# Optimization experiments

Hardware: AMD Instinct MI355X
Metric: run time of the kernel (lower is better)

## Reference

```python
import jax, jax.numpy as jnp
import numpy as np

# dims: T=max seq len, B=batch, D=d_embed, H=d_hidden, NR=n_roles, NH=n_heads
T, B, D, H = 512, 64, 512, 1024
NR, NH = 64, 8
HD = H // NH  # per-head hidden


def _lengths():
    # monotonically non-increasing lengths -> valid PackedSequence batch_sizes
    return np.round(np.linspace(T, T // 4, B)).astype(np.int32)


def _packed_idx(lengths):
    batch_sizes = np.array([(lengths > t).sum() for t in range(T)], dtype=np.int64)
    # flat row index into padded [T*B] for each packed token (time-major)
    return np.concatenate([t * B + np.arange(batch_sizes[t]) for t in range(T)]).astype(np.int32)


def setup_inputs() -> dict:
    key = jax.random.key(0)
    ks = jax.random.split(key, 12)
    lengths = _lengths()
    idx = _packed_idx(lengths)
    total = int(idx.shape[0])  # 20480
    s = lambda k, shape, sc=1.0: (jax.random.normal(k, shape, jnp.float32) * sc)
    return {
        'x': s(ks[0], (total, D)),
        'idx': jnp.asarray(idx),
        'lengths': jnp.asarray(lengths),
        'basis0': s(ks[1], (NR, H)),  # frozen role basis (requires_grad=False)
        'basis1': s(ks[2], (NR, H)),
        'Wx0': s(ks[3], (2 * H, D), 0.02), 'bx0': jnp.zeros((2 * H,), jnp.float32),
        'Wh0': s(ks[4], (2 * H, H), 0.02), 'bh0': jnp.zeros((2 * H,), jnp.float32),
        'Wv0': s(ks[5], (2 * H, H), 0.02), 'bv0': jnp.zeros((2 * H,), jnp.float32),
        'Wx1': s(ks[6], (2 * H, H), 0.02), 'bx1': jnp.zeros((2 * H,), jnp.float32),
        'Wh1': s(ks[7], (2 * H, H), 0.02), 'bh1': jnp.zeros((2 * H,), jnp.float32),
        'Wv1': s(ks[8], (2 * H, H), 0.02), 'bv1': jnp.zeros((2 * H,), jnp.float32),
    }


def _tpru_layer(x2fg_pad, Wh, bh, r, u, lengths):
    """Run the sequential TPRU recurrence over padded [T,B,2H] precomputed x2fg.

    Replaces the packed per-timestep Python loop (output[p:q] slicing with
    varying batch sizes) with a full-batch lax.scan; rows of padded timesteps
    beyond a sequence's length are computed but never read into output or hn,
    so the math on valid positions is identical.
    """
    h0 = jnp.zeros((B, H), x2fg_pad.dtype)
    hn0 = jnp.zeros((B, H), x2fg_pad.dtype)

    def step(carry, inp):
        h, hn = carry
        x2fg_t, t = inp
        fg = h @ Wh.T + bh + x2fg_t                 # [B, 2H]
        f, g = jnp.split(fg, 2, axis=-1)
        fh = f.reshape(B, NH, HD)
        # unbind: attention over roles per head
        scores = jnp.einsum('bnd,rnd->brn', fh, r)   # [B, NR, NH]
        attn = jax.nn.softmax(scores, axis=1)
        # bind: weighted sum of unbinding vectors
        bind = jnp.einsum('brn,rnd->bnd', attn, u).reshape(B, H)
        gate = jax.nn.sigmoid(g)
        h_new = gate * jnp.tanh(bind) + (1.0 - gate) * h
        # hn captures hidden at each sequence's final valid step
        hn = jnp.where((lengths == t + 1)[:, None], h_new, hn)
        return (h_new, hn), h_new

    (_, hn), hs = jax.lax.scan(step, (h0, hn0), (x2fg_pad, jnp.arange(T)))
    return hs, hn  # hs: [T, B, H]


def reference(x, idx, lengths, basis0, basis1, Wx0, bx0, Wh0, bh0, Wv0, bv0,
              Wx1, bx1, Wh1, bh1, Wv1, bv1):
    # unpack packed data [total, D] into padded [T, B, D]
    x_pad = jnp.zeros((T * B, D), x.dtype).at[idx].set(x).reshape(T, B, D)
    # layer 0
    x2fg = x_pad @ Wx0.T + bx0                       # [T, B, 2H]
    v = (basis0 @ Wv0.T + bv0).reshape(NR, NH, 2 * HD)
    hs, hn0 = _tpru_layer(x2fg, Wh0, bh0, v[..., :HD], v[..., HD:], lengths)
    # layer 1 (input dim is now H)
    x2fg = hs @ Wx1.T + bx1
    v = (basis1 @ Wv1.T + bv1).reshape(NR, NH, 2 * HD)
    hs, hn1 = _tpru_layer(x2fg, Wh1, bh1, v[..., :HD], v[..., HD:], lengths)
    # repack output (time-major packed order, matching PackedSequence.data)
    packed = hs.reshape(T * B, H)[idx]               # [total, H]
    hn = jnp.stack([hn0, hn1])                       # [n_layers, B, H]
    return packed, hn
```

## Files before the change

### kernel.cpp

```cpp
#include <hip/hip_runtime.h>

typedef _Float16 f16;
typedef _Float16 f16x2 __attribute__((ext_vector_type(2)));
typedef _Float16 f16x4 __attribute__((ext_vector_type(4)));
typedef _Float16 f16x8 __attribute__((ext_vector_type(8)));
typedef float    f32x4 __attribute__((ext_vector_type(4)));

#define TT   512
#define BB   64
#define DD   512
#define HH   1024
#define H2   2048
#define NR_  64
#define NH_  8
#define HD_  128
#define MROWS (TT*BB)
#define RWG  64

#define ALOAD32(p)   __hip_atomic_load((p),  __ATOMIC_RELAXED, __HIP_MEMORY_SCOPE_AGENT)
#define ASTORE(p,v)  __hip_atomic_store((p), (v), __ATOMIC_RELAXED, __HIP_MEMORY_SCOPE_AGENT)

__global__ void k_cvt(const float* __restrict__ s, f16* __restrict__ d, int n) {
  int i = blockIdx.x * blockDim.x + threadIdx.x;
  int st = gridDim.x * blockDim.x;
  for (; i < n; i += st) d[i] = (f16)s[i];
}

__global__ void k_scatter(const float* __restrict__ x, const int* __restrict__ idx,
                          f16* __restrict__ xpad, int total) {
  int i = blockIdx.x * blockDim.x + threadIdx.x;
  int st = gridDim.x * blockDim.x;
  int n = total * DD;
  for (; i < n; i += st) {
    int p = i >> 9;
    int j = i & (DD - 1);
    xpad[(size_t)idx[p] * DD + j] = (f16)x[i];
  }
}

__global__ void k_inv(const int* __restrict__ idx, int* __restrict__ inv, int total) {
  int i = blockIdx.x * blockDim.x + threadIdx.x;
  if (i < total) inv[idx[i]] = i;
}

__global__ __launch_bounds__(256)
void k_gemm(const f16* __restrict__ A, const f16* __restrict__ Bw,
            const float* __restrict__ bias, f16* __restrict__ C,
            int N, int K, int Mvalid) {
  __shared__ __align__(16) f16 As[128 * 32];
  __shared__ __align__(16) f16 Bs[128 * 32];
  const int tid  = threadIdx.x;
  const int lane = tid & 63;
  const int wave = tid >> 6;
  const int m0 = blockIdx.y * 128;
  const int n0 = blockIdx.x * 128;
  const int mw = (wave >> 1) * 64;
  const int nw = (wave & 1) * 64;
  const int NT = K >> 5;
  const int c0 = tid * 2;

  float4 pa[2], pb[2];
  auto fetch = [&](int kt) {
#pragma unroll
    for (int i = 0; i < 2; ++i) {
      int c = c0 + i;
      int row = c >> 2, kc = c & 3;
      pa[i] = *(const float4*)&A [(size_t)(m0 + row) * K + kt * 32 + kc * 8];
      pb[i] = *(const float4*)&Bw[(size_t)(n0 + row) * K + kt * 32 + kc * 8];
    }
  };

  f32x4 acc[4][4] = {};
  fetch(0);
  for (int kt = 0; kt < NT; ++kt) {
    __syncthreads();
#pragma unroll
    for (int i = 0; i < 2; ++i) {
      int c = c0 + i;
      *(float4*)&As[c * 8] = pa[i];
      *(float4*)&Bs[c * 8] = pb[i];
    }
    __syncthreads();
    if (kt + 1 < NT) fetch(kt + 1);
    f16x8 af[4], bf[4];
#pragma unroll
    for (int i = 0; i < 4; ++i) {
      af[i] = *(const f16x8*)&As[(mw + i * 16 + (lane & 15)) * 32 + (lane >> 4) * 8];
      bf[i] = *(const f16x8*)&Bs[(nw + i * 16 + (lane & 15)) * 32 + (lane >> 4) * 8];
    }
#pragma unroll
    for (int i = 0; i < 4; ++i)
#pragma unroll
      for (int j = 0; j < 4; ++j)
        acc[i][j] = __builtin_amdgcn_mfma_f32_16x16x32_f16(af[i], bf[j], acc[i][j], 0, 0, 0);
  }

#pragma unroll
  for (int j = 0; j < 4; ++j) {
    int col = n0 + nw + j * 16 + (lane & 15);
    float bv = bias[col];
#pragma unroll
    for (int i = 0; i < 4; ++i) {
#pragma unroll
      for (int r = 0; r < 4; ++r) {
        int row = m0 + mw + i * 16 + (lane >> 4) * 4 + r;
        if (row < Mvalid) C[(size_t)row * N + col] = (f16)(acc[i][j][r] + bv);
      }
    }
  }
}

__global__ __launch_bounds__(512, 2)
void k_rec(const f16* __restrict__ Wh16, const float* __restrict__ bh,
           const f16* __restrict__ v16,  const f16* __restrict__ x2fg,
           f16* __restrict__ hfrag, float* __restrict__ fgbuf,
           f16* __restrict__ hs_out, float* __restrict__ out_packed,
           float* __restrict__ hn_out,
           const int* __restrict__ inv, const int* __restrict__ lgt,
           int* __restrict__ Afl, int* __restrict__ Bfl, int epoch0)
{
  __shared__ __align__(16) f16   Wlds[32 * 2 * 64 * 8];
  __shared__ __align__(16) f16x4 Rq[32 * 64];
  __shared__ __align__(16) f16x4 Uq[16 * 2 * 64];
  __shared__ __align__(16) f32x4 pbuf[8][64];
  __shared__ __align__(16) float fbuf[8][128];
  __shared__ __align__(16) float abuf[8][64];

  const int tid  = threadIdx.x;
  const int lane = tid & 63;
  const int wave = tid >> 6;
  const int wg   = blockIdx.x;
  const int cs   = wg;
  const int rt   = wave & 3;
  const int kh   = wave >> 2;
  const int nh   = wg >> 3;
  const int b    = ((wg & 7) << 3) + wave;
  const int cf   = nh * HD_;

  for (int i = tid; i < 32 * 2 * 64; i += 512) {
    int kk = i >> 7;
    int nt = (i >> 6) & 1;
    int ln = i & 63;
    int col = cs * 32 + nt * 16 + (ln & 15);
    int kg  = kk * 32 + (ln >> 4) * 8;
    *(float4*)&Wlds[(size_t)i * 8] = *(const float4*)&Wh16[(size_t)col * HH + kg];
  }
  for (int e = tid; e < 32 * 64; e += 512) {
    int i = e >> 6, role = e & 63;
    Rq[e] = *(const f16x4*)&v16[(size_t)role * H2 + nh * 256 + 4 * i];
  }
  for (int e = tid; e < 16 * 2 * 64; e += 512) {
    int i = e >> 7, half = (e >> 6) & 1, l = e & 63;
    int r0 = 4 * i + 2 * half;
    const f16* u0 = &v16[(size_t)r0 * H2 + nh * 256 + 128 + 2 * l];
    const f16* u1 = &v16[(size_t)(r0 + 1) * H2 + nh * 256 + 128 + 2 * l];
    f16x4 tv; tv.x = u0[0]; tv.y = u0[1]; tv.z = u1[0]; tv.w = u1[1];
    Uq[e] = tv;
  }
  __syncthreads();

  const int d0 = cf + 2 * lane;
  const float2 bf2 = *(const float2*)&bh[d0];
  const float2 bg2 = *(const float2*)&bh[HH + d0];
  const int lb = lgt[b];
  float ho0 = 0.f, ho1 = 0.f;
  const int pidx = (lane < 4) ? (4 * nh + lane)
                 : (lane < 8) ? (28 + 4 * nh + lane)
                 : wg;
  const size_t hoff = (((size_t)kh * 64 + rt) * 64 + lane) * 16;
  const char* hbase0 = (const char*)hfrag;
  const char* hbase1 = (const char*)hfrag + (size_t)BB * HH * 2;
  unsigned* hw32 = (unsigned*)hfrag;
  const char* fp  = (const char*)fgbuf + (((size_t)b * H2) + d0) * 4;
  const char* gp  = fp + (size_t)HH * 4;

  for (int t = 0; t < TT; ++t) {
    const int e = epoch0 + t + 1;
    const size_t row = (size_t)t * BB + b;
    const f16* xr = x2fg + row * H2;
    f16x2 xf = *(const f16x2*)&xr[d0];
    f16x2 xg = *(const f16x2*)&xr[HH + d0];
    int   p  = inv[row];

    for (;;) {
      int v = ALOAD32(&Bfl[lane]);
      if (__all(v >= e - 1)) break;
      __builtin_amdgcn_s_sleep(1);
    }

    f32x4 acc0 = {0.f, 0.f, 0.f, 0.f}, acc1 = acc0;
    {
      const char* hb0 = ((t & 1) ? hbase0 : hbase1) + hoff;
      float4 hb[16];
#pragma unroll
      for (int j = 0; j < 16; ++j) {
        asm volatile("global_load_dwordx4 %0, %1, off sc0 sc1"
                     : "=v"(hb[j]) : "v"(hb0 + (size_t)j * 4096));
      }
      asm volatile("s_waitcnt vmcnt(0)" ::: "memory");
      __builtin_amdgcn_sched_barrier(0);
#pragma unroll
      for (int j = 0; j < 16; ++j) {
        int kk = kh * 16 + j;
        f16x8 af = __builtin_bit_cast(f16x8, hb[j]);
        f16x8 b0 = *(const f16x8*)&Wlds[((kk * 2 + 0) * 64 + lane) * 8];
        f16x8 b1 = *(const f16x8*)&Wlds[((kk * 2 + 1) * 64 + lane) * 8];
        acc0 = __builtin_amdgcn_mfma_f32_16x16x32_f16(af, b0, acc0, 0, 0, 0);
        acc1 = __builtin_amdgcn_mfma_f32_16x16x32_f16(af, b1, acc1, 0, 0, 0);
      }
    }
    pbuf[wave][lane] = (kh == 0) ? acc1 : acc0;
    __syncthreads();
    {
      f32x4 acc = ((kh == 0) ? acc0 : acc1) + pbuf[wave ^ 4][lane];
      const int col = cs * 32 + kh * 16 + (lane & 15);
      const int r0  = rt * 16 + (lane >> 4) * 4;
#pragma unroll
      for (int r = 0; r < 4; ++r) ASTORE(&fgbuf[(size_t)(r0 + r) * H2 + col], acc[r]);
    }
    __syncthreads();
    if (tid == 0) ASTORE(&Afl[wg], e);

    for (;;) {
      int v = ALOAD32(&Afl[pidx]);
      if (__all((lane >= 8) | (v >= e))) break;
      __builtin_amdgcn_s_sleep(1);
    }

    float2 fv, gv;
    asm volatile("global_load_dwordx2 %0, %1, off sc0 sc1" : "=v"(fv) : "v"(fp));
    asm volatile("global_load_dwordx2 %0, %1, off sc0 sc1" : "=v"(gv) : "v"(gp));
    asm volatile("s_waitcnt vmcnt(0)" ::: "memory");
    __builtin_amdgcn_sched_barrier(0);
    float f0 = fv.x + bf2.x + (float)xf.x;
    float f1 = fv.y + bf2.y + (float)xf.y;
    float g0 = gv.x + bg2.x + (float)xg.x;
    float g1 = gv.y + bg2.y + (float)xg.y;
    *(float2*)&fbuf[wave][2 * lane] = make_float2(f0, f1);
    float s = 0.f;
#pragma unroll
    for (int i = 0; i < 32; ++i) {
      float4 fvv = *(const float4*)&fbuf[wave][4 * i];
      f16x4 rv = Rq[i * 64 + lane];
      s = fmaf(fvv.x, (float)rv.x, s);
      s = fmaf(fvv.y, (float)rv.y, s);
      s = fmaf(fvv.z, (float)rv.z, s);
      s = fmaf(fvv.w, (float)rv.w, s);
    }
    float mx = s;
#pragma unroll
    for (int off = 32; off > 0; off >>= 1) mx = fmaxf(mx, __shfl_xor(mx, off));
    float e2 = expf(s - mx);
    float sum = e2;
#pragma unroll
    for (int off = 32; off > 0; off >>= 1) sum += __shfl_xor(sum, off);
    abuf[wave][lane] = e2 / sum;
    float bd0 = 0.f, bd1 = 0.f;
#pragma unroll
    for (int i = 0; i < 16; ++i) {
      float4 av = *(const float4*)&abuf[wave][4 * i];
      f16x4 u01 = Uq[(i * 2 + 0) * 64 + lane];
      f16x4 u23 = Uq[(i * 2 + 1) * 64 + lane];
      bd0 = fmaf(av.x, (float)u01.x, bd0); bd1 = fmaf(av.x, (float)u01.y, bd1);
      bd0 = fmaf(av.y, (float)u01.z, bd0); bd1 = fmaf(av.y, (float)u01.w, bd1);
      bd0 = fmaf(av.z, (float)u23.x, bd0); bd1 = fmaf(av.z, (float)u23.y, bd1);
      bd0 = fmaf(av.w, (float)u23.z, bd0); bd1 = fmaf(av.w, (float)u23.w, bd1);
    }
    float gt0 = 1.f / (1.f + expf(-g0));
    float gt1 = 1.f / (1.f + expf(-g1));
    float hv0 = gt0 * tanhf(bd0) + (1.f - gt0) * ho0;
    float hv1 = gt1 * tanhf(bd1) + (1.f - gt1) * ho1;
    ho0 = hv0; ho1 = hv1;
    {
      const int k0 = d0;
      unsigned hp = (unsigned)__builtin_bit_cast(unsigned short, (f16)hv0)
                  | ((unsigned)__builtin_bit_cast(unsigned short, (f16)hv1) << 16);
      size_t ui = (((size_t)(k0 >> 5) * 4 + (b >> 4)) * 64
                   + ((b & 15) + (((k0 >> 3) & 3) << 4))) * 4 + ((k0 & 7) >> 1);
      ASTORE(hw32 + (size_t)(t & 1) * (BB * HH / 2) + ui, hp);
    }
    __syncthreads();
    if (tid == 0) ASTORE(&Bfl[wg], e);

    if (hs_out) {
      f16x2 hp2; hp2.x = (f16)ho0; hp2.y = (f16)ho1;
      *(f16x2*)&hs_out[row * HH + d0] = hp2;
    }
    if (out_packed && p >= 0) {
      *(float2*)&out_packed[(size_t)p * HH + d0] = make_float2(ho0, ho1);
    }
    if (lb == t + 1) {
      *(float2*)&hn_out[(size_t)b * HH + d0] = make_float2(ho0, ho1);
    }
  }
}

extern "C" void kernel_launch(void* const* d_in, const int* in_sizes, int n_in,
                              void* d_out, int out_size, void* d_ws, size_t ws_size,
                              hipStream_t stream) {
  const float* x      = (const float*)d_in[0];
  const int*   idx    = (const int*)d_in[1];
  const int*   lgt    = (const int*)d_in[2];
  const float* basis0 = (const float*)d_in[3];
  const float* basis1 = (const float*)d_in[4];
  const float* Wx0 = (const float*)d_in[5];  const float* bx0 = (const float*)d_in[6];
  const float* Wh0 = (const float*)d_in[7];  const float* bh0 = (const float*)d_in[8];
  const float* Wv0 = (const float*)d_in[9];  const float* bv0 = (const float*)d_in[10];
  const float* Wx1 = (const float*)d_in[11]; const float* bx1 = (const float*)d_in[12];
  const float* Wh1 = (const float*)d_in[13]; const float* bh1 = (const float*)d_in[14];
  const float* Wv1 = (const float*)d_in[15]; const float* bv1 = (const float*)d_in[16];
  const int total = in_sizes[1];

  char* ws = (char*)d_ws;
  size_t off = 0;
  auto alloc = [&](size_t bytes) -> void* {
    void* p = (void*)(ws + off);
    off += (bytes + 255) & ~(size_t)255;
    return p;
  };

  int*   Afl     = (int*)alloc(RWG * 4);
  int*   Bfl     = (int*)alloc(RWG * 4);
  int*   inv     = (int*)alloc((size_t)MROWS * 4);
  f16*   xpad    = (f16*)alloc((size_t)MROWS * DD * 2);
  f16*   x2fg    = (f16*)alloc((size_t)MROWS * H2 * 2);
  f16*   hfrag   = (f16*)alloc((size_t)2 * BB * HH * 2);
  float* fgbuf   = (float*)alloc((size_t)BB * H2 * 4);
  f16* Wx0h = (f16*)alloc((size_t)H2 * DD * 2);
  f16* Wh0h = (f16*)alloc((size_t)H2 * HH * 2);
  f16* Wv0h = (f16*)alloc((size_t)H2 * HH * 2);
  f16* Wx1h = (f16*)alloc((size_t)H2 * HH * 2);
  f16* Wh1h = (f16*)alloc((size_t)H2 * HH * 2);
  f16* Wv1h = (f16*)alloc((size_t)H2 * HH * 2);
  f16* bas0h = (f16*)alloc((size_t)128 * HH * 2);
  f16* bas1h = (f16*)alloc((size_t)128 * HH * 2);
  f16* v0h = (f16*)alloc((size_t)NR_ * H2 * 2);
  f16* v1h = (f16*)alloc((size_t)NR_ * H2 * 2);

  float* out = (float*)d_out;
  float* hn0 = out + (size_t)total * HH;
  float* hn1 = hn0 + (size_t)BB * HH;
  f16* hs0 = (f16*)d_out;

  (void)hipMemsetAsync(Afl, 0, RWG * 4, stream);
  (void)hipMemsetAsync(Bfl, 0, RWG * 4, stream);
  (void)hipMemsetAsync(inv, 0xFF, (size_t)MROWS * 4, stream);
  (void)hipMemsetAsync(xpad, 0, (size_t)MROWS * DD * 2, stream);
  (void)hipMemsetAsync(bas0h, 0, (size_t)128 * HH * 2, stream);
  (void)hipMemsetAsync(bas1h, 0, (size_t)128 * HH * 2, stream);
  (void)hipMemsetAsync(hfrag, 0, (size_t)2 * BB * HH * 2, stream);

  k_cvt<<<512, 256, 0, stream>>>(Wx0, Wx0h, H2 * DD);
  k_cvt<<<512, 256, 0, stream>>>(Wh0, Wh0h, H2 * HH);
  k_cvt<<<512, 256, 0, stream>>>(Wv0, Wv0h, H2 * HH);
  k_cvt<<<512, 256, 0, stream>>>(Wx1, Wx1h, H2 * HH);
  k_cvt<<<512, 256, 0, stream>>>(Wh1, Wh1h, H2 * HH);
  k_cvt<<<512, 256, 0, stream>>>(Wv1, Wv1h, H2 * HH);
  k_cvt<<<64, 256, 0, stream>>>(basis0, bas0h, NR_ * HH);
  k_cvt<<<64, 256, 0, stream>>>(basis1, bas1h, NR_ * HH);
  k_scatter<<<2048, 256, 0, stream>>>(x, idx, xpad, total);
  k_inv<<<(total + 255) / 256, 256, 0, stream>>>(idx, inv, total);

  dim3 gv(16, 1);
  k_gemm<<<gv, 256, 0, stream>>>(bas0h, Wv0h, bv0, v0h, H2, HH, NR_);
  k_gemm<<<gv, 256, 0, stream>>>(bas1h, Wv1h, bv1, v1h, H2, HH, NR_);

  dim3 gx(H2 / 128, MROWS / 128);
  k_gemm<<<gx, 256, 0, stream>>>(xpad, Wx0h, bx0, x2fg, H2, DD, MROWS);

  k_rec<<<RWG, 512, 0, stream>>>(Wh0h, bh0, v0h, x2fg, hfrag, fgbuf,
                                 hs0, nullptr, hn0, inv, lgt, Afl, Bfl, 0);

  (void)hipMemsetAsync(hfrag, 0, (size_t)2 * BB * HH * 2, stream);

  k_gemm<<<gx, 256, 0, stream>>>(hs0, Wx1h, bx1, x2fg, H2, HH, MROWS);

  k_rec<<<RWG, 512, 0, stream>>>(Wh1h, bh1, v1h, x2fg, hfrag, fgbuf,
                                 nullptr, out, hn1, inv, lgt, Afl, Bfl, TT);
}
```

Before: 9.800 ms.

## Replace per-workgroup barrier flags with per-wave flags in recurrent kernel

```diff
diff --git a/kernel.cpp b/kernel.cpp
--- a/kernel.cpp
+++ b/kernel.cpp
@@ -122,7 +122,7 @@
   __shared__ __align__(16) f16   Wlds[32 * 2 * 64 * 8];
   __shared__ __align__(16) f16x4 Rq[32 * 64];
   __shared__ __align__(16) f16x4 Uq[16 * 2 * 64];
-  __shared__ __align__(16) f32x4 pbuf[8][64];
+  __shared__ __align__(16) f32x4 pbuf[2][8][64];
   __shared__ __align__(16) float fbuf[8][128];
   __shared__ __align__(16) float abuf[8][64];
 
@@ -164,13 +164,20 @@
   const float2 bg2 = *(const float2*)&bh[HH + d0];
   const int lb = lgt[b];
   float ho0 = 0.f, ho1 = 0.f;
-  const int pidx = (lane < 4) ? (4 * nh + lane)
-                 : (lane < 8) ? (28 + 4 * nh + lane)
-                 : wg;
+  const int myf = wg * 8 + wave;
+  const int rtb = b >> 4;
+  int widx;
+  {
+    int j = lane & 3, gsel = (lane >> 2) & 1, khp = (lane >> 3) & 1;
+    int wgp = (gsel ? 32 : 0) + 4 * nh + j;
+    widx = (lane < 16) ? (wgp * 8 + khp * 4 + rtb) : myf;
+  }
   const size_t hoff = (((size_t)kh * 64 + rt) * 64 + lane) * 16;
   const char* hbase0 = (const char*)hfrag;
   const char* hbase1 = (const char*)hfrag + (size_t)BB * HH * 2;
   unsigned* hw32 = (unsigned*)hfrag;
+  const size_t hui = ((((size_t)(d0 >> 5) * 4 + (b >> 4)) * 64
+                      + ((b & 15) + (((d0 >> 3) & 3) << 4))) * 4 + ((d0 & 7) >> 1));
   const char* fp  = (const char*)fgbuf + (((size_t)b * H2) + d0) * 4;
   const char* gp  = fp + (size_t)HH * 4;
 
@@ -183,8 +190,13 @@
     int   p  = inv[row];
 
     for (;;) {
-      int v = ALOAD32(&Bfl[lane]);
-      if (__all(v >= e - 1)) break;
+      int ok = 1;
+#pragma unroll
+      for (int j = 0; j < 4; ++j) {
+        int v = ALOAD32(&Bfl[256 * kh + j * 64 + lane]);
+        ok &= (v >= e - 1);
+      }
+      if (__all(ok)) break;
       __builtin_amdgcn_s_sleep(1);
     }
 
@@ -209,21 +221,22 @@
         acc1 = __builtin_amdgcn_mfma_f32_16x16x32_f16(af, b1, acc1, 0, 0, 0);
       }
     }
-    pbuf[wave][lane] = (kh == 0) ? acc1 : acc0;
+    pbuf[t & 1][wave][lane] = (kh == 0) ? acc1 : acc0;
     __syncthreads();
     {
-      f32x4 acc = ((kh == 0) ? acc0 : acc1) + pbuf[wave ^ 4][lane];
+      f32x4 acc = ((kh == 0) ? acc0 : acc1) + pbuf[t & 1][wave ^ 4][lane];
       const int col = cs * 32 + kh * 16 + (lane & 15);
       const int r0  = rt * 16 + (lane >> 4) * 4;
 #pragma unroll
       for (int r = 0; r < 4; ++r) ASTORE(&fgbuf[(size_t)(r0 + r) * H2 + col], acc[r]);
     }
-    __syncthreads();
-    if (tid == 0) ASTORE(&Afl[wg], e);
+    asm volatile("s_waitcnt vmcnt(0)" ::: "memory");
+    __builtin_amdgcn_sched_barrier(0);
+    if (lane == 0) ASTORE(&Afl[myf], e);
 
     for (;;) {
-      int v = ALOAD32(&Afl[pidx]);
-      if (__all((lane >= 8) | (v >= e))) break;
+      int v = ALOAD32(&Afl[widx]);
+      if (__all(v >= e)) break;
       __builtin_amdgcn_s_sleep(1);
     }
 
@@ -272,15 +285,13 @@
     float hv1 = gt1 * tanhf(bd1) + (1.f - gt1) * ho1;
     ho0 = hv0; ho1 = hv1;
     {
-      const int k0 = d0;
       unsigned hp = (unsigned)__builtin_bit_cast(unsigned short, (f16)hv0)
                   | ((unsigned)__builtin_bit_cast(unsigned short, (f16)hv1) << 16);
-      size_t ui = (((size_t)(k0 >> 5) * 4 + (b >> 4)) * 64
-                   + ((b & 15) + (((k0 >> 3) & 3) << 4))) * 4 + ((k0 & 7) >> 1);
-      ASTORE(hw32 + (size_t)(t & 1) * (BB * HH / 2) + ui, hp);
-    }
-    __syncthreads();
-    if (tid == 0) ASTORE(&Bfl[wg], e);
+      ASTORE(hw32 + (size_t)(t & 1) * (BB * HH / 2) + hui, hp);
+    }
+    asm volatile("s_waitcnt vmcnt(0)" ::: "memory");
+    __builtin_amdgcn_sched_barrier(0);
+    if (lane == 0) ASTORE(&Bfl[myf], e);
 
     if (hs_out) {
       f16x2 hp2; hp2.x = (f16)ho0; hp2.y = (f16)ho1;
@@ -319,8 +330,8 @@
     return p;
   };
 
-  int*   Afl     = (int*)alloc(RWG * 4);
-  int*   Bfl     = (int*)alloc(RWG * 4);
+  int*   Afl     = (int*)alloc(RWG * 8 * 4);
+  int*   Bfl     = (int*)alloc(RWG * 8 * 4);
   int*   inv     = (int*)alloc((size_t)MROWS * 4);
   f16*   xpad    = (f16*)alloc((size_t)MROWS * DD * 2);
   f16*   x2fg    = (f16*)alloc((size_t)MROWS * H2 * 2);
@@ -342,8 +353,8 @@
   float* hn1 = hn0 + (size_t)BB * HH;
   f16* hs0 = (f16*)d_out;
 
-  (void)hipMemsetAsync(Afl, 0, RWG * 4, stream);
-  (void)hipMemsetAsync(Bfl, 0, RWG * 4, stream);
+  (void)hipMemsetAsync(Afl, 0, RWG * 8 * 4, stream);
+  (void)hipMemsetAsync(Bfl, 0, RWG * 8 * 4, stream);
   (void)hipMemsetAsync(inv, 0xFF, (size_t)MROWS * 4, stream);
   (void)hipMemsetAsync(xpad, 0, (size_t)MROWS * DD * 2, stream);
   (void)hipMemsetAsync(bas0h, 0, (size_t)128 * HH * 2, stream);
```

New measurement: 14.47 ms. +47.6%, slower.
